# Kernel optimization log

Measured on AMD Instinct MI355X. Metric: run time of the kernel, lower is better.

The kernel has to match this reference:

```python
import jax, jax.numpy as jnp
import numpy as np

N_NODES = 100000

def graph_conv(x, src, dst, W_rel, W_root, b, num_nodes):
    # PyG GraphConv: out_i = lin_rel(sum_{j in N(i)} x_j) + lin_root(x_i)
    agg = jax.ops.segment_sum(x[src], dst, num_segments=num_nodes)  # [N, F_in]
    return agg @ W_rel + x @ W_root + b


def setup_inputs() -> dict:
    key = jax.random.key(0)
    ks = jax.random.split(key, 8)
    z = jax.random.normal(ks[0], (N_NODES, 64), dtype=jnp.float32)
    edge_index = jax.random.randint(ks[1], (2, 1600000), 0, N_NODES, dtype=jnp.int64)
    def glorot(k, fi, fo):
        s = (6.0 / (fi + fo)) ** 0.5
        return jax.random.uniform(k, (fi, fo), dtype=jnp.float32, minval=-s, maxval=s)
    return {
        "z": z,
        "edge_index": edge_index,
        "W_rel1": glorot(ks[2], 64, 32), "W_root1": glorot(ks[3], 64, 32), "b1": jnp.zeros((32,), jnp.float32),
        "W_rel2": glorot(ks[4], 32, 16), "W_root2": glorot(ks[5], 32, 16), "b2": jnp.zeros((16,), jnp.float32),
        "W_rel3": glorot(ks[6], 16, 2), "W_root3": glorot(ks[7], 16, 2), "b3": jnp.zeros((2,), jnp.float32),
    }


def reference(z, edge_index, W_rel1, W_root1, b1, W_rel2, W_root2, b2, W_rel3, W_root3, b3):
    src, dst = edge_index[0], edge_index[1]
    h = graph_conv(z, src, dst, W_rel1, W_root1, b1, N_NODES)
    h = jax.nn.relu(h)
    h = graph_conv(h, src, dst, W_rel2, W_root2, b2, N_NODES)
    h = jax.nn.relu(h)
    h = graph_conv(h, src, dst, W_rel3, W_root3, b3, N_NODES)
    return jax.nn.softmax(h, axis=-1)
```

## Files before the change

### kernel.cpp

```cpp
#include <hip/hip_runtime.h>
#include <hip/hip_bf16.h>


#define RNODES 128
#define NB_MAX 1024
#define CH 4096
#define CMAX 512

template <int Fin, int Fout, bool RELU>
__global__ void linear2_kernel(const float* __restrict__ x,
                               const float* __restrict__ Wrel,
                               const float* __restrict__ Wroot,
                               const float* __restrict__ bias,
                               float* __restrict__ t,
                               float* __restrict__ acc, int N) {
    const bool rootTask = (blockIdx.y != 0);
    const float* __restrict__ W = rootTask ? Wroot : Wrel;
    float* __restrict__ outp    = rootTask ? acc : t;

    int n = blockIdx.x * blockDim.x + threadIdx.x;
    if (n >= N) return;

    float o[Fout];
#pragma unroll
    for (int f = 0; f < Fout; ++f) o[f] = 0.f;

    const float* xr = x + (size_t)n * Fin;
    for (int k0 = 0; k0 < Fin; k0 += 16) {
#pragma unroll
        for (int k = 0; k < 16; k += 4) {
            float4 v = *(const float4*)(xr + k0 + k);
            if (RELU) {
                v.x = fmaxf(v.x, 0.f); v.y = fmaxf(v.y, 0.f);
                v.z = fmaxf(v.z, 0.f); v.w = fmaxf(v.w, 0.f);
            }
            const float xv[4] = {v.x, v.y, v.z, v.w};
#pragma unroll
            for (int kk = 0; kk < 4; ++kk) {
                const float* wr = W + (size_t)(k0 + k + kk) * Fout;
#pragma unroll
                for (int f = 0; f < Fout; ++f)
                    o[f] = fmaf(xv[kk], wr[f], o[f]);
            }
        }
    }
    if (rootTask) {
#pragma unroll
        for (int f = 0; f < Fout; ++f) o[f] += bias[f];
    }
    float* op = outp + (size_t)n * Fout;
    if constexpr (Fout >= 4) {
#pragma unroll
        for (int f = 0; f < Fout; f += 4)
            *(float4*)(op + f) = make_float4(o[f], o[f + 1], o[f + 2], o[f + 3]);
    } else {
        *(float2*)op = make_float2(o[0], o[1]);
    }
}

__global__ void hist_chunked_kernel(const int* __restrict__ dst,
                                    int* __restrict__ chunkhist,
                                    int nE, int NB) {
    __shared__ int h[NB_MAX];
    const int c  = blockIdx.x;
    const int e0 = c * CH, e1 = min(e0 + CH, nE);
    for (int b = threadIdx.x; b < NB; b += blockDim.x) h[b] = 0;
    __syncthreads();
    for (int e = e0 + threadIdx.x; e < e1; e += blockDim.x)
        atomicAdd(&h[dst[e] >> 7], 1);
    __syncthreads();
    for (int b = threadIdx.x; b < NB; b += blockDim.x)
        chunkhist[(size_t)c * NB + b] = h[b];
}

__global__ void scan_chunkhist_kernel(int* __restrict__ chunkhist,
                                      int* __restrict__ gtotal,
                                      int C, int NB) {
    __shared__ int s[CMAX];
    const int b = blockIdx.x;
    const int t = threadIdx.x;
    int v = (t < C) ? chunkhist[(size_t)t * NB + b] : 0;
    s[t] = v;
    __syncthreads();
    for (int off = 1; off < CMAX; off <<= 1) {
        int u = (t >= off) ? s[t - off] : 0;
        __syncthreads();
        s[t] += u;
        __syncthreads();
    }
    if (t < C) chunkhist[(size_t)t * NB + b] = s[t] - v;
    if (t == CMAX - 1) gtotal[b] = s[t];
}

__global__ void scan_buckets_kernel(const int* __restrict__ gtotal,
                                    int* __restrict__ bptr, int NB, int nE) {
    __shared__ int s[NB_MAX];
    int t = threadIdx.x;
    int own = (t < NB) ? gtotal[t] : 0;
    s[t] = own;
    __syncthreads();
    for (int off = 1; off < NB_MAX; off <<= 1) {
        int v = (t >= off) ? s[t - off] : 0;
        __syncthreads();
        s[t] += v;
        __syncthreads();
    }
    if (t < NB) bptr[t] = s[t] - own;
    if (t == 0) bptr[NB] = nE;
}

__global__ void bucketize_det_kernel(const int* __restrict__ src,
                                     const int* __restrict__ dst,
                                     const int* __restrict__ chunkpre,
                                     const int* __restrict__ bptr,
                                     unsigned int* __restrict__ records,
                                     int nE, int NB) {
    __shared__ int lcur[NB_MAX];
    const int c  = blockIdx.x;
    const int e0 = c * CH, e1 = min(e0 + CH, nE);
    for (int b = threadIdx.x; b < NB; b += blockDim.x)
        lcur[b] = bptr[b] + chunkpre[(size_t)c * NB + b];
    __syncthreads();
    for (int e = e0 + threadIdx.x; e < e1; e += blockDim.x) {
        int d = dst[e];
        int b = d >> 7;
        int pos = atomicAdd(&lcur[b], 1);
        records[pos] = (unsigned int)src[e] | ((unsigned int)(d & 127) << 17);
    }
}

__global__ void place_merge_kernel(const unsigned int* __restrict__ records,
                                   const int* __restrict__ bptr,
                                   int* __restrict__ rowptr,
                                   int* __restrict__ srcs_sorted,
                                   int N, int nE, int NB) {
    __shared__ int hist[RNODES];
    __shared__ int s[RNODES];
    __shared__ int lcur[RNODES];
    const int b    = blockIdx.x;
    const int base = b * RNODES;
    const int nn   = min(RNODES, N - base);
    const int beg  = bptr[b], end = bptr[b + 1];
    const int t    = threadIdx.x;

    if (t < RNODES) hist[t] = 0;
    __syncthreads();
    for (int i = beg + t; i < end; i += blockDim.x)
        atomicAdd(&hist[records[i] >> 17], 1);
    __syncthreads();

    if (t < RNODES) s[t] = hist[t];
    __syncthreads();
    for (int off = 1; off < RNODES; off <<= 1) {
        int v = (t < RNODES && t >= off) ? s[t - off] : 0;
        __syncthreads();
        if (t < RNODES && t >= off) s[t] += v;
        __syncthreads();
    }
    if (t < nn) {
        int ex = beg + s[t] - hist[t];
        rowptr[base + t] = ex;
        lcur[t] = ex;
    }
    if (b == NB - 1 && t == 0) rowptr[N] = nE;
    __syncthreads();

    for (int i = beg + t; i < end; i += blockDim.x) {
        unsigned int rec = records[i];
        int pos = atomicAdd(&lcur[rec >> 17], 1);
        srcs_sorted[pos] = (int)(rec & 0x1FFFFu);
    }
}

template <int F, bool SOFTMAX>
__global__ void gather_agg_kernel(const float* __restrict__ t,
                                  const int* __restrict__ rowptr,
                                  const int* __restrict__ srcs,
                                  const float* __restrict__ rootacc,
                                  float* __restrict__ out, int N) {
    int tid = blockIdx.x * blockDim.x + threadIdx.x;
    int n = tid / F;
    if (n >= N) return;
    int f = tid & (F - 1);
    const float* tf = t + f;
    int beg = rowptr[n], end = rowptr[n + 1];
    float sum = 0.0f;
    int e = beg;
    for (; e + 16 <= end; e += 16) {
        int s[16];
        float v[16];
#pragma unroll
        for (int u = 0; u < 16; ++u) s[u] = srcs[e + u];
#pragma unroll
        for (int u = 0; u < 16; ++u) v[u] = tf[(long)s[u] * F];
#pragma unroll
        for (int u = 0; u < 16; ++u) sum += v[u];
    }
    for (; e + 4 <= end; e += 4) {
        int s[4];
        float v[4];
#pragma unroll
        for (int u = 0; u < 4; ++u) s[u] = srcs[e + u];
#pragma unroll
        for (int u = 0; u < 4; ++u) v[u] = tf[(long)s[u] * F];
        sum += (v[0] + v[1]) + (v[2] + v[3]);
    }
    for (; e < end; ++e) sum += tf[(long)srcs[e] * F];

    float v = rootacc[(long)n * F + f] + sum;
    if (!SOFTMAX) {
        out[(long)n * F + f] = v;
    } else {
        float o = __shfl_xor(v, 1, 64);
        float m = fmaxf(v, o);
        float ev = __expf(v - m), eo = __expf(o - m);
        out[(long)n * F + f] = ev / (ev + eo);
    }
}

template <int F>
__global__ void scatter_kernel(const float* __restrict__ t,
                               const int* __restrict__ src,
                               const int* __restrict__ dst,
                               float* __restrict__ acc, int nE) {
    int tid = blockIdx.x * blockDim.x + threadIdx.x;
    int e = tid / F;
    if (e >= nE) return;
    int f = tid & (F - 1);
    atomicAdd(acc + (long)dst[e] * F + f, t[(long)src[e] * F + f]);
}

__global__ void softmax2_kernel(const float* __restrict__ h, float* __restrict__ out, int N) {
    int n = blockIdx.x * blockDim.x + threadIdx.x;
    if (n >= N) return;
    float a = h[2 * n], b = h[2 * n + 1];
    float m = fmaxf(a, b);
    float ea = __expf(a - m), eb = __expf(b - m);
    float inv = 1.0f / (ea + eb);
    out[2 * n] = ea * inv;
    out[2 * n + 1] = eb * inv;
}

extern "C" void kernel_launch(void* const* d_in, const int* in_sizes, int n_in,
                              void* d_out, int out_size, void* d_ws, size_t ws_size,
                              hipStream_t stream) {
    const float* z      = (const float*)d_in[0];
    const int*   ei     = (const int*)d_in[1];
    const float* Wrel1  = (const float*)d_in[2];
    const float* Wroot1 = (const float*)d_in[3];
    const float* b1     = (const float*)d_in[4];
    const float* Wrel2  = (const float*)d_in[5];
    const float* Wroot2 = (const float*)d_in[6];
    const float* b2     = (const float*)d_in[7];
    const float* Wrel3  = (const float*)d_in[8];
    const float* Wroot3 = (const float*)d_in[9];
    const float* b3     = (const float*)d_in[10];

    const int N  = in_sizes[0] / 64;
    const int nE = in_sizes[1] / 2;
    const int* src = ei;
    const int* dst = ei + nE;
    const int NB = (N + RNODES - 1) / RNODES;
    const int C  = (nE + CH - 1) / CH;

    float* regionA = (float*)d_ws;
    float* regionB = regionA + (size_t)N * 32;
    float* t1 = regionA;
    float* h1 = regionB;
    float* t2 = regionA;
    float* h2 = regionA + (size_t)N * 16;
    float* t3 = regionB;
    float* h3 = regionB + (size_t)N * 2;
    unsigned int* records = (unsigned int*)regionA;

    int* chunkhist = (int*)regionB;
    int* gtotal    = chunkhist + (size_t)CMAX * NB_MAX;
    int* bptr      = gtotal + NB_MAX;
    int* ibase       = (int*)(regionB + (size_t)N * 32);
    int* rowptr      = ibase;
    int* srcs_sorted = rowptr + N + 1;

    size_t needed = (size_t)N * 64 * sizeof(float)
                  + ((size_t)N + 1 + (size_t)nE) * sizeof(int);
    size_t buildNeed = ((size_t)CMAX * NB_MAX + NB_MAX + NB_MAX + 1) * sizeof(int);

    const int B = 256;
    const int nodeBlocks = (N + B - 1) / B;
    const dim3 linGrid(nodeBlocks, 2);
    const bool packOK = (N <= (1 << 17)) && (NB <= NB_MAX) && (C <= CMAX)
                      && ((size_t)nE * 4 <= (size_t)N * 32 * 4)
                      && (buildNeed <= (size_t)N * 32 * 4);

    if (ws_size >= needed && packOK) {
        hist_chunked_kernel<<<C, 512, 0, stream>>>(dst, chunkhist, nE, NB);
        scan_chunkhist_kernel<<<NB, CMAX, 0, stream>>>(chunkhist, gtotal, C, NB);
        scan_buckets_kernel<<<1, NB_MAX, 0, stream>>>(gtotal, bptr, NB, nE);
        bucketize_det_kernel<<<C, 512, 0, stream>>>(src, dst, chunkhist, bptr, records, nE, NB);
        place_merge_kernel<<<NB, 512, 0, stream>>>(records, bptr, rowptr, srcs_sorted, N, nE, NB);

        linear2_kernel<64, 32, false><<<linGrid, B, 0, stream>>>(z, Wrel1, Wroot1, b1, t1, h1, N);
        gather_agg_kernel<32, false><<<((size_t)N * 32 + B - 1) / B, B, 0, stream>>>(
            t1, rowptr, srcs_sorted, h1, h1, N);

        linear2_kernel<32, 16, true><<<linGrid, B, 0, stream>>>(h1, Wrel2, Wroot2, b2, t2, h2, N);
        gather_agg_kernel<16, false><<<((size_t)N * 16 + B - 1) / B, B, 0, stream>>>(
            t2, rowptr, srcs_sorted, h2, h2, N);

        linear2_kernel<16, 2, true><<<linGrid, B, 0, stream>>>(h2, Wrel3, Wroot3, b3, t3, h3, N);
        gather_agg_kernel<2, true><<<((size_t)N * 2 + B - 1) / B, B, 0, stream>>>(
            t3, rowptr, srcs_sorted, h3, (float*)d_out, N);
    } else {
        linear2_kernel<64, 32, false><<<linGrid, B, 0, stream>>>(z, Wrel1, Wroot1, b1, t1, h1, N);
        scatter_kernel<32><<<((size_t)nE * 32 + B - 1) / B, B, 0, stream>>>(t1, src, dst, h1, nE);
        linear2_kernel<32, 16, true><<<linGrid, B, 0, stream>>>(h1, Wrel2, Wroot2, b2, t2, h2, N);
        scatter_kernel<16><<<((size_t)nE * 16 + B - 1) / B, B, 0, stream>>>(t2, src, dst, h2, nE);
        linear2_kernel<16, 2, true><<<linGrid, B, 0, stream>>>(h2, Wrel3, Wroot3, b3, t3, h3, N);
        scatter_kernel<2><<<((size_t)nE * 2 + B - 1) / B, B, 0, stream>>>(t3, src, dst, h3, nE);
        softmax2_kernel<<<nodeBlocks, B, 0, stream>>>(h3, (float*)d_out, N);
    }
}
```

Measured before the change: 248.7 us.

## Fuse next-layer linear transforms into gather-aggregate kernels and re-lay workspace

Each gather-aggregation kernel now also applies ReLU and the next layer's rel/root linear transforms through shared memory, producing the next layer's t and root-accumulator directly. This removes two linear2 launches and the write and re-read of the intermediate h1/h2 activations. The workspace is laid out sequentially with separate buffers instead of aliased regions, which increases workspace need and drops the aliasing-size constraints from the fast-path check. Each thread in the fused kernel now holds 32 weight registers, which may reduce occupancy in the gather loop.

```diff
diff --git a/kernel.cpp b/kernel.cpp
--- a/kernel.cpp
+++ b/kernel.cpp
@@ -6,6 +6,35 @@
 #define NB_MAX 1024
 #define CH 4096
 #define CMAX 512
+
+template <int F>
+__device__ __forceinline__ float gather_sum(const float* __restrict__ tf,
+                                            const int* __restrict__ srcs,
+                                            int beg, int end) {
+    float sum = 0.0f;
+    int e = beg;
+    for (; e + 16 <= end; e += 16) {
+        int s[16];
+        float v[16];
+#pragma unroll
+        for (int u = 0; u < 16; ++u) s[u] = srcs[e + u];
+#pragma unroll
+        for (int u = 0; u < 16; ++u) v[u] = tf[(long)s[u] * F];
+#pragma unroll
+        for (int u = 0; u < 16; ++u) sum += v[u];
+    }
+    for (; e + 4 <= end; e += 4) {
+        int s[4];
+        float v[4];
+#pragma unroll
+        for (int u = 0; u < 4; ++u) s[u] = srcs[e + u];
+#pragma unroll
+        for (int u = 0; u < 4; ++u) v[u] = tf[(long)s[u] * F];
+        sum += (v[0] + v[1]) + (v[2] + v[3]);
+    }
+    for (; e < end; ++e) sum += tf[(long)srcs[e] * F];
+    return sum;
+}
 
 template <int Fin, int Fout, bool RELU>
 __global__ void linear2_kernel(const float* __restrict__ x,
@@ -172,50 +201,95 @@
     }
 }
 
-template <int F, bool SOFTMAX>
-__global__ void gather_agg_kernel(const float* __restrict__ t,
-                                  const int* __restrict__ rowptr,
-                                  const int* __restrict__ srcs,
-                                  const float* __restrict__ rootacc,
-                                  float* __restrict__ out, int N) {
+__global__ void gather_fuse32_kernel(const float* __restrict__ t1,
+                                     const int* __restrict__ rowptr,
+                                     const int* __restrict__ srcs,
+                                     const float* __restrict__ h1root,
+                                     const float* __restrict__ W2rel,
+                                     const float* __restrict__ W2root,
+                                     const float* __restrict__ b2,
+                                     float* __restrict__ t2,
+                                     float* __restrict__ h2root, int N) {
+    __shared__ float sx[256];
+    const int tid = blockIdx.x * blockDim.x + threadIdx.x;
+    const int n = tid >> 5;
+    const int f = tid & 31;
+    const bool valid = (n < N);
+
+    float v = 0.f;
+    if (valid) {
+        int beg = rowptr[n], end = rowptr[n + 1];
+        v = h1root[(size_t)n * 32 + f] + gather_sum<32>(t1 + f, srcs, beg, end);
+    }
+    sx[threadIdx.x] = fmaxf(v, 0.f);
+
+    const int g = f & 15;
+    const float* Wc = (f < 16) ? W2rel : W2root;
+    float wcol[32];
+#pragma unroll
+    for (int k = 0; k < 32; ++k) wcol[k] = Wc[k * 16 + g];
+    __syncthreads();
+
+    if (valid) {
+        const float* xs = &sx[threadIdx.x & ~31];
+        float o = 0.f;
+#pragma unroll
+        for (int k = 0; k < 32; ++k) o = fmaf(xs[k], wcol[k], o);
+        if (f < 16) t2[(size_t)n * 16 + g] = o;
+        else        h2root[(size_t)n * 16 + g] = o + b2[g];
+    }
+}
+
+__global__ void gather_fuse16_kernel(const float* __restrict__ t2,
+                                     const int* __restrict__ rowptr,
+                                     const int* __restrict__ srcs,
+                                     const float* __restrict__ h2root,
+                                     const float* __restrict__ W3rel,
+                                     const float* __restrict__ W3root,
+                                     const float* __restrict__ b3,
+                                     float* __restrict__ t3,
+                                     float* __restrict__ h3root, int N) {
+    __shared__ float sx[256];
+    const int tid = blockIdx.x * blockDim.x + threadIdx.x;
+    const int n = tid >> 4;
+    const int f = tid & 15;
+    const bool valid = (n < N);
+
+    float v = 0.f;
+    if (valid) {
+        int beg = rowptr[n], end = rowptr[n + 1];
+        v = h2root[(size_t)n * 16 + f] + gather_sum<16>(t2 + f, srcs, beg, end);
+    }
+    sx[threadIdx.x] = fmaxf(v, 0.f);
+    __syncthreads();
+
+    if (valid && f < 4) {
+        const int g = f & 1;
+        const float* Wc = (f < 2) ? W3rel : W3root;
+        const float* xs = &sx[threadIdx.x & ~15];
+        float o = 0.f;
+#pragma unroll
+        for (int k = 0; k < 16; ++k) o = fmaf(xs[k], Wc[k * 2 + g], o);
+        if (f < 2) t3[(size_t)n * 2 + g] = o;
+        else       h3root[(size_t)n * 2 + g] = o + b3[g];
+    }
+}
+
+__global__ void gather_softmax2_kernel(const float* __restrict__ t3,
+                                       const int* __restrict__ rowptr,
+                                       const int* __restrict__ srcs,
+                                       const float* __restrict__ h3root,
+                                       float* __restrict__ out, int N) {
     int tid = blockIdx.x * blockDim.x + threadIdx.x;
-    int n = tid / F;
+    int n = tid >> 1;
     if (n >= N) return;
-    int f = tid & (F - 1);
-    const float* tf = t + f;
+    int f = tid & 1;
     int beg = rowptr[n], end = rowptr[n + 1];
-    float sum = 0.0f;
-    int e = beg;
-    for (; e + 16 <= end; e += 16) {
-        int s[16];
-        float v[16];
-#pragma unroll
-        for (int u = 0; u < 16; ++u) s[u] = srcs[e + u];
-#pragma unroll
-        for (int u = 0; u < 16; ++u) v[u] = tf[(long)s[u] * F];
-#pragma unroll
-        for (int u = 0; u < 16; ++u) sum += v[u];
-    }
-    for (; e + 4 <= end; e += 4) {
-        int s[4];
-        float v[4];
-#pragma unroll
-        for (int u = 0; u < 4; ++u) s[u] = srcs[e + u];
-#pragma unroll
-        for (int u = 0; u < 4; ++u) v[u] = tf[(long)s[u] * F];
-        sum += (v[0] + v[1]) + (v[2] + v[3]);
-    }
-    for (; e < end; ++e) sum += tf[(long)srcs[e] * F];
-
-    float v = rootacc[(long)n * F + f] + sum;
-    if (!SOFTMAX) {
-        out[(long)n * F + f] = v;
-    } else {
-        float o = __shfl_xor(v, 1, 64);
-        float m = fmaxf(v, o);
-        float ev = __expf(v - m), eo = __expf(o - m);
-        out[(long)n * F + f] = ev / (ev + eo);
-    }
+    float v = h3root[(size_t)n * 2 + f] + gather_sum<2>(t3 + f, srcs, beg, end);
+    float o = __shfl_xor(v, 1, 64);
+    float m = fmaxf(v, o);
+    float ev = __expf(v - m), eo = __expf(o - m);
+    out[(size_t)n * 2 + f] = ev / (ev + eo);
 }
 
 template <int F>
@@ -263,33 +337,25 @@
     const int NB = (N + RNODES - 1) / RNODES;
     const int C  = (nE + CH - 1) / CH;
 
-    float* regionA = (float*)d_ws;
-    float* regionB = regionA + (size_t)N * 32;
-    float* t1 = regionA;
-    float* h1 = regionB;
-    float* t2 = regionA;
-    float* h2 = regionA + (size_t)N * 16;
-    float* t3 = regionB;
-    float* h3 = regionB + (size_t)N * 2;
-    unsigned int* records = (unsigned int*)regionA;
-
-    int* chunkhist = (int*)regionB;
-    int* gtotal    = chunkhist + (size_t)CMAX * NB_MAX;
-    int* bptr      = gtotal + NB_MAX;
-    int* ibase       = (int*)(regionB + (size_t)N * 32);
-    int* rowptr      = ibase;
-    int* srcs_sorted = rowptr + N + 1;
-
-    size_t needed = (size_t)N * 64 * sizeof(float)
-                  + ((size_t)N + 1 + (size_t)nE) * sizeof(int);
-    size_t buildNeed = ((size_t)CMAX * NB_MAX + NB_MAX + NB_MAX + 1) * sizeof(int);
+    char* p = (char*)d_ws;
+    unsigned int* records = (unsigned int*)p;  p += (size_t)nE * 4;
+    int* chunkhist = (int*)p;                  p += (size_t)CMAX * NB_MAX * 4;
+    int* gtotal    = (int*)p;                  p += (size_t)NB_MAX * 4;
+    int* bptr      = (int*)p;                  p += ((size_t)NB_MAX + 1) * 4;
+    int* rowptr    = (int*)p;                  p += ((size_t)N + 1) * 4;
+    int* srcs_sorted = (int*)p;                p += (size_t)nE * 4;
+    float* t1     = (float*)p;                 p += (size_t)N * 32 * 4;
+    float* h1root = (float*)p;                 p += (size_t)N * 32 * 4;
+    float* t2     = (float*)p;                 p += (size_t)N * 16 * 4;
+    float* h2root = (float*)p;                 p += (size_t)N * 16 * 4;
+    float* t3     = (float*)p;                 p += (size_t)N * 2 * 4;
+    float* h3root = (float*)p;                 p += (size_t)N * 2 * 4;
+    size_t needed = (size_t)(p - (char*)d_ws);
 
     const int B = 256;
     const int nodeBlocks = (N + B - 1) / B;
     const dim3 linGrid(nodeBlocks, 2);
-    const bool packOK = (N <= (1 << 17)) && (NB <= NB_MAX) && (C <= CMAX)
-                      && ((size_t)nE * 4 <= (size_t)N * 32 * 4)
-                      && (buildNeed <= (size_t)N * 32 * 4);
+    const bool packOK = (N <= (1 << 17)) && (NB <= NB_MAX) && (C <= CMAX);
 
     if (ws_size >= needed && packOK) {
         hist_chunked_kernel<<<C, 512, 0, stream>>>(dst, chunkhist, nE, NB);
@@ -298,24 +364,24 @@
         bucketize_det_kernel<<<C, 512, 0, stream>>>(src, dst, chunkhist, bptr, records, nE, NB);
         place_merge_kernel<<<NB, 512, 0, stream>>>(records, bptr, rowptr, srcs_sorted, N, nE, NB);
 
-        linear2_kernel<64, 32, false><<<linGrid, B, 0, stream>>>(z, Wrel1, Wroot1, b1, t1, h1, N);
-        gather_agg_kernel<32, false><<<((size_t)N * 32 + B - 1) / B, B, 0, stream>>>(
-            t1, rowptr, srcs_sorted, h1, h1, N);
-
-        linear2_kernel<32, 16, true><<<linGrid, B, 0, stream>>>(h1, Wrel2, Wroot2, b2, t2, h2, N);
-        gather_agg_kernel<16, false><<<((size_t)N * 16 + B - 1) / B, B, 0, stream>>>(
-            t2, rowptr, srcs_sorted, h2, h2, N);
-
-        linear2_kernel<16, 2, true><<<linGrid, B, 0, stream>>>(h2, Wrel3, Wroot3, b3, t3, h3, N);
-        gather_agg_kernel<2, true><<<((size_t)N * 2 + B - 1) / B, B, 0, stream>>>(
-            t3, rowptr, srcs_sorted, h3, (float*)d_out, N);
+        linear2_kernel<64, 32, false><<<linGrid, B, 0, stream>>>(
+            z, Wrel1, Wroot1, b1, t1, h1root, N);
+
+        gather_fuse32_kernel<<<((size_t)N * 32 + B - 1) / B, B, 0, stream>>>(
+            t1, rowptr, srcs_sorted, h1root, Wrel2, Wroot2, b2, t2, h2root, N);
+
+        gather_fuse16_kernel<<<((size_t)N * 16 + B - 1) / B, B, 0, stream>>>(
+            t2, rowptr, srcs_sorted, h2root, Wrel3, Wroot3, b3, t3, h3root, N);
+
+        gather_softmax2_kernel<<<((size_t)N * 2 + B - 1) / B, B, 0, stream>>>(
+            t3, rowptr, srcs_sorted, h3root, (float*)d_out, N);
     } else {
-        linear2_kernel<64, 32, false><<<linGrid, B, 0, stream>>>(z, Wrel1, Wroot1, b1, t1, h1, N);
-        scatter_kernel<32><<<((size_t)nE * 32 + B - 1) / B, B, 0, stream>>>(t1, src, dst, h1, nE);
-        linear2_kernel<32, 16, true><<<linGrid, B, 0, stream>>>(h1, Wrel2, Wroot2, b2, t2, h2, N);
-        scatter_kernel<16><<<((size_t)nE * 16 + B - 1) / B, B, 0, stream>>>(t2, src, dst, h2, nE);
-        linear2_kernel<16, 2, true><<<linGrid, B, 0, stream>>>(h2, Wrel3, Wroot3, b3, t3, h3, N);
-        scatter_kernel<2><<<((size_t)nE * 2 + B - 1) / B, B, 0, stream>>>(t3, src, dst, h3, nE);
-        softmax2_kernel<<<nodeBlocks, B, 0, stream>>>(h3, (float*)d_out, N);
-    }
-}
+        linear2_kernel<64, 32, false><<<linGrid, B, 0, stream>>>(z, Wrel1, Wroot1, b1, t1, h1root, N);
+        scatter_kernel<32><<<((size_t)nE * 32 + B - 1) / B, B, 0, stream>>>(t1, src, dst, h1root, nE);
+        linear2_kernel<32, 16, true><<<linGrid, B, 0, stream>>>(h1root, Wrel2, Wroot2, b2, t2, h2root, N);
+        scatter_kernel<16><<<((size_t)nE * 16 + B - 1) / B, B, 0, stream>>>(t2, src, dst, h2root, nE);
+        linear2_kernel<16, 2, true><<<linGrid, B, 0, stream>>>(h2root, Wrel3, Wroot3, b3, t3, h3root, N);
+        scatter_kernel<2><<<((size_t)nE * 2 + B - 1) / B, B, 0, stream>>>(t3, src, dst, h3root, nE);
+        softmax2_kernel<<<nodeBlocks, B, 0, stream>>>(h3root, (float*)d_out, N);
+    }
+}
```

New measurement: 268.1 us. 1.08x slower.

## Fuse layer-1 linear transform with destination histogram into one launch

Applied to the files above, without the earlier changes.

Merges the first-layer dual linear kernel and the chunked destination histogram into a single heterogeneous kernel whose blocks pick either task by block index. This lets the independent histogram run alongside the dense matmul and removes one launch. To make that possible, the CSR build scratch (records, chunk histograms, bucket pointers) moves out of regions reused by t1/h1 into a dedicated tail of the workspace. The workspace requirement grows, and the histogram now runs with 256-thread blocks instead of 512.

```diff
diff --git a/kernel.cpp b/kernel.cpp
--- a/kernel.cpp
+++ b/kernel.cpp
@@ -6,6 +6,64 @@
 #define NB_MAX 1024
 #define CH 4096
 #define CMAX 512
+
+template <int Fin, int Fout>
+__global__ void lin1_hist_kernel(const float* __restrict__ x,
+                                 const float* __restrict__ Wrel,
+                                 const float* __restrict__ Wroot,
+                                 const float* __restrict__ bias,
+                                 float* __restrict__ t,
+                                 float* __restrict__ acc, int N,
+                                 const int* __restrict__ dst,
+                                 int* __restrict__ chunkhist,
+                                 int nE, int NB, int nodeBlocks) {
+    __shared__ int h[NB_MAX];
+    const int bx = blockIdx.x;
+    if (bx < 2 * nodeBlocks) {
+        const bool rootTask = (bx >= nodeBlocks);
+        const float* __restrict__ W = rootTask ? Wroot : Wrel;
+        float* __restrict__ outp    = rootTask ? acc : t;
+        int n = (rootTask ? bx - nodeBlocks : bx) * blockDim.x + threadIdx.x;
+        if (n >= N) return;
+
+        float o[Fout];
+#pragma unroll
+        for (int f = 0; f < Fout; ++f) o[f] = 0.f;
+        const float* xr = x + (size_t)n * Fin;
+        for (int k0 = 0; k0 < Fin; k0 += 16) {
+#pragma unroll
+            for (int k = 0; k < 16; k += 4) {
+                float4 v = *(const float4*)(xr + k0 + k);
+                const float xv[4] = {v.x, v.y, v.z, v.w};
+#pragma unroll
+                for (int kk = 0; kk < 4; ++kk) {
+                    const float* wr = W + (size_t)(k0 + k + kk) * Fout;
+#pragma unroll
+                    for (int f = 0; f < Fout; ++f)
+                        o[f] = fmaf(xv[kk], wr[f], o[f]);
+                }
+            }
+        }
+        if (rootTask) {
+#pragma unroll
+            for (int f = 0; f < Fout; ++f) o[f] += bias[f];
+        }
+        float* op = outp + (size_t)n * Fout;
+#pragma unroll
+        for (int f = 0; f < Fout; f += 4)
+            *(float4*)(op + f) = make_float4(o[f], o[f + 1], o[f + 2], o[f + 3]);
+    } else {
+        const int c  = bx - 2 * nodeBlocks;
+        const int e0 = c * CH, e1 = min(e0 + CH, nE);
+        for (int b = threadIdx.x; b < NB; b += blockDim.x) h[b] = 0;
+        __syncthreads();
+        for (int e = e0 + threadIdx.x; e < e1; e += blockDim.x)
+            atomicAdd(&h[dst[e] >> 7], 1);
+        __syncthreads();
+        for (int b = threadIdx.x; b < NB; b += blockDim.x)
+            chunkhist[(size_t)c * NB + b] = h[b];
+    }
+}
 
 template <int Fin, int Fout, bool RELU>
 __global__ void linear2_kernel(const float* __restrict__ x,
@@ -56,21 +114,6 @@
     } else {
         *(float2*)op = make_float2(o[0], o[1]);
     }
-}
-
-__global__ void hist_chunked_kernel(const int* __restrict__ dst,
-                                    int* __restrict__ chunkhist,
-                                    int nE, int NB) {
-    __shared__ int h[NB_MAX];
-    const int c  = blockIdx.x;
-    const int e0 = c * CH, e1 = min(e0 + CH, nE);
-    for (int b = threadIdx.x; b < NB; b += blockDim.x) h[b] = 0;
-    __syncthreads();
-    for (int e = e0 + threadIdx.x; e < e1; e += blockDim.x)
-        atomicAdd(&h[dst[e] >> 7], 1);
-    __syncthreads();
-    for (int b = threadIdx.x; b < NB; b += blockDim.x)
-        chunkhist[(size_t)c * NB + b] = h[b];
 }
 
 __global__ void scan_chunkhist_kernel(int* __restrict__ chunkhist,
@@ -271,34 +314,32 @@
     float* h2 = regionA + (size_t)N * 16;
     float* t3 = regionB;
     float* h3 = regionB + (size_t)N * 2;
-    unsigned int* records = (unsigned int*)regionA;
-
-    int* chunkhist = (int*)regionB;
-    int* gtotal    = chunkhist + (size_t)CMAX * NB_MAX;
-    int* bptr      = gtotal + NB_MAX;
+
     int* ibase       = (int*)(regionB + (size_t)N * 32);
     int* rowptr      = ibase;
     int* srcs_sorted = rowptr + N + 1;
+    unsigned int* records = (unsigned int*)(srcs_sorted + nE);
+    int* chunkhist   = (int*)(records + nE);
+    int* gtotal      = chunkhist + (size_t)CMAX * NB_MAX;
+    int* bptr        = gtotal + NB_MAX;
 
     size_t needed = (size_t)N * 64 * sizeof(float)
-                  + ((size_t)N + 1 + (size_t)nE) * sizeof(int);
-    size_t buildNeed = ((size_t)CMAX * NB_MAX + NB_MAX + NB_MAX + 1) * sizeof(int);
+                  + ((size_t)N + 1 + 2 * (size_t)nE
+                     + (size_t)CMAX * NB_MAX + 2 * NB_MAX + 1) * sizeof(int);
 
     const int B = 256;
     const int nodeBlocks = (N + B - 1) / B;
     const dim3 linGrid(nodeBlocks, 2);
-    const bool packOK = (N <= (1 << 17)) && (NB <= NB_MAX) && (C <= CMAX)
-                      && ((size_t)nE * 4 <= (size_t)N * 32 * 4)
-                      && (buildNeed <= (size_t)N * 32 * 4);
+    const bool packOK = (N <= (1 << 17)) && (NB <= NB_MAX) && (C <= CMAX);
 
     if (ws_size >= needed && packOK) {
-        hist_chunked_kernel<<<C, 512, 0, stream>>>(dst, chunkhist, nE, NB);
+        lin1_hist_kernel<64, 32><<<2 * nodeBlocks + C, B, 0, stream>>>(
+            z, Wrel1, Wroot1, b1, t1, h1, N, dst, chunkhist, nE, NB, nodeBlocks);
         scan_chunkhist_kernel<<<NB, CMAX, 0, stream>>>(chunkhist, gtotal, C, NB);
         scan_buckets_kernel<<<1, NB_MAX, 0, stream>>>(gtotal, bptr, NB, nE);
         bucketize_det_kernel<<<C, 512, 0, stream>>>(src, dst, chunkhist, bptr, records, nE, NB);
         place_merge_kernel<<<NB, 512, 0, stream>>>(records, bptr, rowptr, srcs_sorted, N, nE, NB);
 
-        linear2_kernel<64, 32, false><<<linGrid, B, 0, stream>>>(z, Wrel1, Wroot1, b1, t1, h1, N);
         gather_agg_kernel<32, false><<<((size_t)N * 32 + B - 1) / B, B, 0, stream>>>(
             t1, rowptr, srcs_sorted, h1, h1, N);
 
```

Result: no change. 249.2 us (+0.2%).
